# Kernel optimization log

Hardware: AMD Instinct MI355X
Metric: run time of the kernel (lower is better)

Reference implementation:

```python
import jax, jax.numpy as jnp
import numpy as np


def _pack_ternary(codes):
    # codes: [N, K] uint8 in {0,1,2} (encoded = ternary_value + 1)
    N, K = codes.shape
    c = codes.reshape(N, K // 4, 4).astype(np.uint8)
    shifts = np.array([0, 2, 4, 6], dtype=np.uint8)
    packed = (c << shifts).sum(axis=-1).astype(np.uint8)
    return packed  # [N, K//4]


def setup_inputs() -> dict:
    key = jax.random.key(0)
    k1, k2 = jax.random.split(key)
    M, K, N = 8192, 4096, 4096
    x = jax.random.normal(k1, (M, K), dtype=jnp.float16)
    # valid INT2 packed ternary weights: 2-bit fields in {0,1,2} = value+1
    codes = np.asarray(jax.random.randint(k2, (N, K), 0, 3), dtype=np.uint8)
    W_packed = jnp.asarray(_pack_ternary(codes), dtype=jnp.uint8)
    gamma = jnp.ones((1,), dtype=jnp.float32)
    return {"x": x, "W_packed": W_packed, "gamma": gamma}


def _unpack_w(W_packed, K):
    # W_packed: [N, K//4] uint8 -> ternary float32 W: [N, K]
    N = W_packed.shape[0]
    shifts = jnp.array([0, 2, 4, 6], dtype=jnp.uint8)
    fields = (W_packed[:, :, None] >> shifts) & jnp.uint8(3)  # [N, K//4, 4]
    w = fields.reshape(N, -1)[:, :K].astype(jnp.float32) - 1.0  # {-1,0,1}
    return w


def reference(x, W_packed, gamma):
    K = x.shape[-1]
    W = _unpack_w(W_packed, K)  # [N, K] ternary
    # Y = X @ W.T * gamma (kernel does fp16 TC GEMM with inline dequant scale)
    Xf = x.astype(jnp.float32)
    Y = jnp.einsum('mk,nk->mn', Xf, W) * gamma[0]
    return Y.astype(jnp.float16)
```

## Files before the change

### kernel.cpp

```cpp
#include <hip/hip_runtime.h>
#include <cstdint>
#include <cstddef>

#define M_DIM 8192
#define N_DIM 4096
#define K_DIM 4096

typedef _Float16 f16x8 __attribute__((ext_vector_type(8)));
typedef float f32x4 __attribute__((ext_vector_type(4)));
typedef unsigned short ushort8 __attribute__((ext_vector_type(8)));

#define GLOAD_LDS16(g, l)                                                      \
  __builtin_amdgcn_global_load_lds(                                            \
      (const __attribute__((address_space(1))) void*)(g),                      \
      (__attribute__((address_space(3))) void*)(l), 16, 0, 0)

__device__ inline uint32_t lutf16(uint32_t c) {
  return (c == 1u) ? 0u : (0x3C00u | ((uint32_t)(c == 0u) << 15));
}

__global__ __launch_bounds__(256) void prep_x(const float4* __restrict__ X,
                                              ushort8* __restrict__ Xf) {
  int i = blockIdx.x * 256 + threadIdx.x;
  float4 f0 = X[2 * (size_t)i], f1 = X[2 * (size_t)i + 1];
  ushort8 us;
  us[0] = __builtin_bit_cast(uint16_t, (_Float16)f0.x);
  us[1] = __builtin_bit_cast(uint16_t, (_Float16)f0.y);
  us[2] = __builtin_bit_cast(uint16_t, (_Float16)f0.z);
  us[3] = __builtin_bit_cast(uint16_t, (_Float16)f0.w);
  us[4] = __builtin_bit_cast(uint16_t, (_Float16)f1.x);
  us[5] = __builtin_bit_cast(uint16_t, (_Float16)f1.y);
  us[6] = __builtin_bit_cast(uint16_t, (_Float16)f1.z);
  us[7] = __builtin_bit_cast(uint16_t, (_Float16)f1.w);
  Xf[i] = us;
}

__global__ __launch_bounds__(256) void prep_w(const uint2* __restrict__ W,
                                              uint4* __restrict__ Wf) {
  int i = blockIdx.x * 256 + threadIdx.x;
  uint2 wv = W[(size_t)i];
  uint32_t x = wv.x & 0xFFu, y = wv.y & 0xFFu;
  uint4 o;
  o.x = lutf16(x & 3u) | (lutf16((x >> 2) & 3u) << 16);
  o.y = lutf16((x >> 4) & 3u) | (lutf16((x >> 6) & 3u) << 16);
  o.z = lutf16(y & 3u) | (lutf16((y >> 2) & 3u) << 16);
  o.w = lutf16((y >> 4) & 3u) | (lutf16((y >> 6) & 3u) << 16);
  Wf[i] = o;
}

__global__ __launch_bounds__(512, 2) void gemm8(
    const _Float16* __restrict__ A,
    const _Float16* __restrict__ B,
    const float* __restrict__ G,
    float* __restrict__ C) {
  __shared__ __align__(16) _Float16 As[2][16384];
  __shared__ __align__(16) _Float16 Bs[2][16384];

  const int tid = threadIdx.x;
  const int wid = tid >> 6;
  const int lane = tid & 63;
  const int wr = wid >> 2;
  const int wcq = wid & 3;
  const int fr = lane & 15, kg = lane >> 4;

  int bid = (int)blockIdx.x;
  int swz = ((bid & 7) << 6) | (bid >> 3);
  const int bm = (swz >> 4) * 256;
  const int bn = (swz & 15) * 256;

  const int sr8 = lane >> 3;
  const int scol = ((lane & 7) ^ sr8) * 8;

  f32x4 acc[8][4] = {};
  f16x8 bfr[4][2];
  f16x8 af0[2][2], af1[2][2];

#define STAGE(t, ht)                                                           \
  do {                                                                         \
    const int buf_ = (t) & 1;                                                  \
    const int kt_ = (t) << 6;                                                  \
    const _Float16* src_ =                                                     \
        ((ht) < 2) ? (B + (size_t)bn * K_DIM) : (A + (size_t)bm * K_DIM);      \
    _Float16* dst_ = ((ht) < 2) ? Bs[buf_] : As[buf_];                         \
    const int h_ = (ht) & 1;                                                   \
    _Pragma("unroll") for (int j_ = 0; j_ < 2; ++j_) {                         \
      int sg_ = h_ * 16 + wid * 2 + j_;                                        \
      int row_ = sg_ * 8 + sr8;                                                \
      GLOAD_LDS16(src_ + (size_t)row_ * K_DIM + kt_ + scol, dst_ + sg_ * 512); \
    }                                                                          \
  } while (0)

#define STAGE_FULL(t)                                                          \
  do { STAGE(t, 0); STAGE(t, 1); STAGE(t, 2); STAGE(t, 3); } while (0)

#define READ_B(t)                                                              \
  do {                                                                         \
    const int buf_ = (t) & 1;                                                  \
    _Pragma("unroll") for (int ni_ = 0; ni_ < 4; ++ni_)                        \
        _Pragma("unroll") for (int ks_ = 0; ks_ < 2; ++ks_) {                  \
      int row_ = wcq * 64 + ni_ * 16 + fr;                                     \
      bfr[ni_][ks_] = *reinterpret_cast<const f16x8*>(                         \
          Bs[buf_] + row_ * 64 + (((ks_ * 4 + kg) ^ (row_ & 7)) * 8));         \
    }                                                                          \
  } while (0)

#define READ_A(t, q, dst)                                                      \
  do {                                                                         \
    const int buf_ = (t) & 1;                                                  \
    _Pragma("unroll") for (int m2_ = 0; m2_ < 2; ++m2_)                        \
        _Pragma("unroll") for (int ks_ = 0; ks_ < 2; ++ks_) {                  \
      int row_ = wr * 128 + ((q) * 2 + m2_) * 16 + fr;                         \
      dst[m2_][ks_] = *reinterpret_cast<const f16x8*>(                         \
          As[buf_] + row_ * 64 + (((ks_ * 4 + kg) ^ (row_ & 7)) * 8));         \
    }                                                                          \
  } while (0)

#define MFMA_Q(q, src)                                                         \
  do {                                                                         \
    __builtin_amdgcn_s_setprio(1);                                             \
    _Pragma("unroll") for (int m2_ = 0; m2_ < 2; ++m2_)                        \
        _Pragma("unroll") for (int ni_ = 0; ni_ < 4; ++ni_)                    \
            _Pragma("unroll") for (int ks_ = 0; ks_ < 2; ++ks_)                \
                acc[(q) * 2 + m2_][ni_] =                                      \
        __builtin_amdgcn_mfma_f32_16x16x32_f16(                                \
            src[m2_][ks_], bfr[ni_][ks_], acc[(q) * 2 + m2_][ni_], 0, 0, 0);   \
    __builtin_amdgcn_s_setprio(0);                                             \
  } while (0)

#define VM0() asm volatile("s_waitcnt vmcnt(0)" ::: "memory")

#define TILE(t, LAST)                                                          \
  do {                                                                         \
    VM0();                                                                     \
    __builtin_amdgcn_s_barrier();                                              \
    if (!(LAST)) STAGE_FULL((t) + 1);                                          \
    READ_B(t);                                                                 \
    READ_A(t, 0, af0);                                                         \
    READ_A(t, 1, af1);             \
    MFMA_Q(0, af0);                                                            \
    READ_A(t, 2, af0);                                   \
    MFMA_Q(1, af1);                                                            \
    READ_A(t, 3, af1);                                   \
    MFMA_Q(2, af0);                                                            \
    MFMA_Q(3, af1);                                                            \
  } while (0)

  STAGE_FULL(0);
  for (int t = 0; t < 63; ++t) TILE(t, false);
  TILE(63, true);

#undef STAGE
#undef STAGE_FULL
#undef READ_B
#undef READ_A
#undef MFMA_Q
#undef VM0
#undef TILE

  float g = G[0];
  if (!(__builtin_fabsf(g) >= 0.001f && __builtin_fabsf(g) <= 1000.0f)) g = 1.0f;
#pragma unroll
  for (int m = 0; m < 8; ++m)
#pragma unroll
    for (int ni = 0; ni < 4; ++ni) {
      int col = bn + wcq * 64 + ni * 16 + fr;
      int row0 = bm + wr * 128 + m * 16 + kg * 4;
#pragma unroll
      for (int j = 0; j < 4; ++j)
        C[(size_t)(row0 + j) * N_DIM + col] = acc[m][ni][j] * g;
    }
}

__global__ __launch_bounds__(256) void gemm_inline(
    const float* __restrict__ X, const uint32_t* __restrict__ W,
    const float* __restrict__ G, float* __restrict__ C) {
  __shared__ __align__(16) _Float16 As[128 * 64];
  __shared__ __align__(16) _Float16 Bs[128 * 64];

  const int tid = threadIdx.x;
  const int wave = tid >> 6;
  const int lane = tid & 63;
  const int wr = wave >> 1, wc = wave & 1;
  const int fr = lane & 15, kg = lane >> 4;
  const int bm = blockIdx.y * 128, bn = blockIdx.x * 128;
  const int brow = tid >> 1, bhalf = tid & 1;

  f32x4 acc[4][4] = {};

  for (int kt = 0; kt < K_DIM; kt += 64) {
#pragma unroll
    for (int i = 0; i < 4; ++i) {
      int c = i * 256 + tid;
      int row = c >> 3, cc = c & 7;
      const float4* p =
          (const float4*)(X + (size_t)(bm + row) * K_DIM + kt + cc * 8);
      float4 f0 = p[0], f1 = p[1];
      ushort8 us;
      us[0] = __builtin_bit_cast(uint16_t, (_Float16)f0.x);
      us[1] = __builtin_bit_cast(uint16_t, (_Float16)f0.y);
      us[2] = __builtin_bit_cast(uint16_t, (_Float16)f0.z);
      us[3] = __builtin_bit_cast(uint16_t, (_Float16)f0.w);
      us[4] = __builtin_bit_cast(uint16_t, (_Float16)f1.x);
      us[5] = __builtin_bit_cast(uint16_t, (_Float16)f1.y);
      us[6] = __builtin_bit_cast(uint16_t, (_Float16)f1.z);
      us[7] = __builtin_bit_cast(uint16_t, (_Float16)f1.w);
      *reinterpret_cast<ushort8*>((uint16_t*)As + row * 64 +
                                  (cc ^ (row & 7)) * 8) = us;
    }
    {
      const uint32_t* wp =
          W + (size_t)(bn + brow) * 1024 + (kt >> 2) + bhalf * 8;
      uint32_t w[8];
      *(uint4*)(w) = *(const uint4*)(wp);
      *(uint4*)(w + 4) = *(const uint4*)(wp + 4);
#pragma unroll
      for (int q = 0; q < 4; ++q) {
        uint32_t x = w[2 * q] & 0xFFu, y = w[2 * q + 1] & 0xFFu;
        uint4 o;
        o.x = lutf16(x & 3u) | (lutf16((x >> 2) & 3u) << 16);
        o.y = lutf16((x >> 4) & 3u) | (lutf16((x >> 6) & 3u) << 16);
        o.z = lutf16(y & 3u) | (lutf16((y >> 2) & 3u) << 16);
        o.w = lutf16((y >> 4) & 3u) | (lutf16((y >> 6) & 3u) << 16);
        int slot = (bhalf * 4 + q) ^ (brow & 7);
        *reinterpret_cast<uint4*>((uint16_t*)Bs + brow * 64 + slot * 8) = o;
      }
    }
    __syncthreads();

#pragma unroll
    for (int ks = 0; ks < 2; ++ks) {
      f16x8 a[4], b[4];
#pragma unroll
      for (int r = 0; r < 4; ++r) {
        int row = wr * 64 + r * 16 + fr;
        a[r] = *reinterpret_cast<const f16x8*>(
            As + row * 64 + ((ks * 4 + kg) ^ (row & 7)) * 8);
      }
#pragma unroll
      for (int c = 0; c < 4; ++c) {
        int row = wc * 64 + c * 16 + fr;
        b[c] = *reinterpret_cast<const f16x8*>(
            Bs + row * 64 + ((ks * 4 + kg) ^ (row & 7)) * 8);
      }
#pragma unroll
      for (int r = 0; r < 4; ++r)
#pragma unroll
        for (int c = 0; c < 4; ++c)
          acc[r][c] = __builtin_amdgcn_mfma_f32_16x16x32_f16(a[r], b[c],
                                                             acc[r][c], 0, 0, 0);
    }
    __syncthreads();
  }

  float g = G[0];
  if (!(__builtin_fabsf(g) >= 0.001f && __builtin_fabsf(g) <= 1000.0f)) g = 1.0f;
#pragma unroll
  for (int r = 0; r < 4; ++r)
#pragma unroll
    for (int c = 0; c < 4; ++c) {
      int col = bn + wc * 64 + c * 16 + fr;
      int row0 = bm + wr * 64 + r * 16 + kg * 4;
#pragma unroll
      for (int j = 0; j < 4; ++j)
        C[(size_t)(row0 + j) * N_DIM + col] = acc[r][c][j] * g;
    }
}

extern "C" void kernel_launch(void* const* d_in, const int* in_sizes, int n_in,
                              void* d_out, int out_size, void* d_ws,
                              size_t ws_size, hipStream_t stream) {
  const float* x = (const float*)d_in[0];
  const uint32_t* w32 = (const uint32_t*)d_in[1];
  const float* gamma = (const float*)d_in[2];
  float* out = (float*)d_out;
  (void)in_sizes; (void)n_in; (void)out_size;

  const size_t xf_bytes = (size_t)M_DIM * K_DIM * 2;
  const size_t wf_bytes = (size_t)N_DIM * K_DIM * 2;

  if (ws_size >= xf_bytes + wf_bytes) {
    _Float16* xf = (_Float16*)d_ws;
    _Float16* wf = (_Float16*)((char*)d_ws + xf_bytes);
    prep_x<<<M_DIM * K_DIM / 8 / 256, 256, 0, stream>>>((const float4*)x,
                                                        (ushort8*)xf);
    prep_w<<<N_DIM * K_DIM / 8 / 256, 256, 0, stream>>>((const uint2*)w32,
                                                        (uint4*)wf);
    gemm8<<<(M_DIM / 256) * (N_DIM / 256), 512, 0, stream>>>(xf, wf, gamma,
                                                             out);
  } else {
    dim3 grid(N_DIM / 128, M_DIM / 128);
    gemm_inline<<<grid, 256, 0, stream>>>(x, w32, gamma, out);
  }
}
```

Measured before the change: 297.0 us.

## Software-pipeline LDS fragment reads across K tiles with double-buffered B registers

Restructures the main GEMM K loop into a two-tile unrolled software pipeline. The next tile's A and B fragments are read from LDS while the current tile's MFMAs run, using two B fragment register sets and mid-tile barriers, so there is no stall on LDS reads at each tile start. It also drops the s_setprio around MFMA groups and reorders the MFMA loops to ks-outer. The cost is more registers and extra barriers, and there is a risk of buffer overwrite races given the two-stage LDS ring.

```diff
diff --git a/kernel.cpp b/kernel.cpp
--- a/kernel.cpp
+++ b/kernel.cpp
@@ -72,8 +72,8 @@
   const int scol = ((lane & 7) ^ sr8) * 8;
 
   f32x4 acc[8][4] = {};
-  f16x8 bfr[4][2];
-  f16x8 af0[2][2], af1[2][2];
+  f16x8 bf0[4][2], bf1[4][2];
+  f16x8 afA[2][2], afB[2][2];
 
 #define STAGE(t, ht)                                                           \
   do {                                                                         \
@@ -93,13 +93,13 @@
 #define STAGE_FULL(t)                                                          \
   do { STAGE(t, 0); STAGE(t, 1); STAGE(t, 2); STAGE(t, 3); } while (0)
 
-#define READ_B(t)                                                              \
+#define READ_B(t, dst)                                                         \
   do {                                                                         \
     const int buf_ = (t) & 1;                                                  \
     _Pragma("unroll") for (int ni_ = 0; ni_ < 4; ++ni_)                        \
         _Pragma("unroll") for (int ks_ = 0; ks_ < 2; ++ks_) {                  \
       int row_ = wcq * 64 + ni_ * 16 + fr;                                     \
-      bfr[ni_][ks_] = *reinterpret_cast<const f16x8*>(                         \
+      dst[ni_][ks_] = *reinterpret_cast<const f16x8*>(                         \
           Bs[buf_] + row_ * 64 + (((ks_ * 4 + kg) ^ (row_ & 7)) * 8));         \
     }                                                                          \
   } while (0)
@@ -115,60 +115,79 @@
     }                                                                          \
   } while (0)
 
-#define MFMA_Q(q, src)                                                         \
+#define MFMA_Q(q, asrc, bsrc)                                                  \
   do {                                                                         \
-    __builtin_amdgcn_s_setprio(1);                                             \
-    _Pragma("unroll") for (int m2_ = 0; m2_ < 2; ++m2_)                        \
-        _Pragma("unroll") for (int ni_ = 0; ni_ < 4; ++ni_)                    \
-            _Pragma("unroll") for (int ks_ = 0; ks_ < 2; ++ks_)                \
+    _Pragma("unroll") for (int ks_ = 0; ks_ < 2; ++ks_)                        \
+        _Pragma("unroll") for (int m2_ = 0; m2_ < 2; ++m2_)                    \
+            _Pragma("unroll") for (int ni_ = 0; ni_ < 4; ++ni_)                \
                 acc[(q) * 2 + m2_][ni_] =                                      \
         __builtin_amdgcn_mfma_f32_16x16x32_f16(                                \
-            src[m2_][ks_], bfr[ni_][ks_], acc[(q) * 2 + m2_][ni_], 0, 0, 0);   \
-    __builtin_amdgcn_s_setprio(0);                                             \
+            asrc[m2_][ks_], bsrc[ni_][ks_], acc[(q) * 2 + m2_][ni_], 0, 0, 0); \
   } while (0)
 
+#define BAR() __builtin_amdgcn_s_barrier()
+#define VM8() asm volatile("s_waitcnt vmcnt(8)" ::: "memory")
 #define VM0() asm volatile("s_waitcnt vmcnt(0)" ::: "memory")
 
-#define TILE(t, LAST)                                                          \
-  do {                                                                         \
-    VM0();                                                                     \
-    __builtin_amdgcn_s_barrier();                                              \
-    if (!(LAST)) STAGE_FULL((t) + 1);                                          \
-    READ_B(t);                                                                 \
-    READ_A(t, 0, af0);                                                         \
-    READ_A(t, 1, af1);             \
-    MFMA_Q(0, af0);                                                            \
-    READ_A(t, 2, af0);                                   \
-    MFMA_Q(1, af1);                                                            \
-    READ_A(t, 3, af1);                                   \
-    MFMA_Q(2, af0);                                                            \
-    MFMA_Q(3, af1);                                                            \
-  } while (0)
-
   STAGE_FULL(0);
-  for (int t = 0; t < 63; ++t) TILE(t, false);
-  TILE(63, true);
-
+  STAGE_FULL(1);
+  VM8();
+  BAR();
+  READ_B(0, bf0);
+  READ_A(0, 0, afA);
+  READ_A(0, 1, afB);
+
+  for (int i = 0; i < 31; ++i) {
+    const int t = 2 * i;
+    MFMA_Q(0, afA, bf0); READ_A(t, 2, afA);
+    MFMA_Q(1, afB, bf0); READ_A(t, 3, afB);
+    VM0(); BAR();
+    STAGE_FULL(t + 2);
+    READ_B(t + 1, bf1);
+    MFMA_Q(2, afA, bf0); READ_A(t + 1, 0, afA);
+    MFMA_Q(3, afB, bf0); READ_A(t + 1, 1, afB);
+    BAR();
+    MFMA_Q(0, afA, bf1); READ_A(t + 1, 2, afA);
+    MFMA_Q(1, afB, bf1); READ_A(t + 1, 3, afB);
+    VM0(); BAR();
+    STAGE_FULL(t + 3);
+    READ_B(t + 2, bf0);
+    MFMA_Q(2, afA, bf1); READ_A(t + 2, 0, afA);
+    MFMA_Q(3, afB, bf1); READ_A(t + 2, 1, afB);
+    BAR();
+  }
+  MFMA_Q(0, afA, bf0); READ_A(62, 2, afA);
+  MFMA_Q(1, afB, bf0); READ_A(62, 3, afB);
+  VM0(); BAR();
+  READ_B(63, bf1);
+  MFMA_Q(2, afA, bf0); READ_A(63, 0, afA);
+  MFMA_Q(3, afB, bf0); READ_A(63, 1, afB);
+  BAR();
+  MFMA_Q(0, afA, bf1); READ_A(63, 2, afA);
+  MFMA_Q(1, afB, bf1); READ_A(63, 3, afB);
+  MFMA_Q(2, afA, bf1);
+  MFMA_Q(3, afB, bf1);
+
+  float g = G[0];
+  if (!(__builtin_fabsf(g) >= 0.001f && __builtin_fabsf(g) <= 1000.0f)) g = 1.0f;
+#pragma unroll
+  for (int m = 0; m < 8; ++m)
+#pragma unroll
+    for (int ni = 0; ni < 4; ++ni) {
+      int col = bn + wcq * 64 + ni * 16 + fr;
+      int row0 = bm + wr * 128 + m * 16 + kg * 4;
+#pragma unroll
+      for (int j = 0; j < 4; ++j)
+        C[(size_t)(row0 + j) * N_DIM + col] = acc[m][ni][j] * g;
+    }
 #undef STAGE
 #undef STAGE_FULL
 #undef READ_B
 #undef READ_A
 #undef MFMA_Q
+#undef BAR
+#undef VM8
 #undef VM0
-#undef TILE
-
-  float g = G[0];
-  if (!(__builtin_fabsf(g) >= 0.001f && __builtin_fabsf(g) <= 1000.0f)) g = 1.0f;
-#pragma unroll
-  for (int m = 0; m < 8; ++m)
-#pragma unroll
-    for (int ni = 0; ni < 4; ++ni) {
-      int col = bn + wcq * 64 + ni * 16 + fr;
-      int row0 = bm + wr * 128 + m * 16 + kg * 4;
-#pragma unroll
-      for (int j = 0; j < 4; ++j)
-        C[(size_t)(row0 + j) * N_DIM + col] = acc[m][ni][j] * g;
-    }
 }
 
 __global__ __launch_bounds__(256) void gemm_inline(
```

Result: faster. 286.8 us (-3.4%).
